# Kernel optimization log

Measured on AMD Instinct MI355X. Metric: run time of the kernel, lower is better.

## Reference

```python
import jax, jax.numpy as jnp
import numpy as np

B, V, T, C, HIN, WIN = 1, 6, 3, 256, 32, 32
NH = 8
LN_EPS = 1e-5


def setup_inputs() -> dict:
    key = jax.random.key(0)
    ks = jax.random.split(key, 14)
    s = 0.02
    lim = 1.0 / np.sqrt(C)
    def lin_w(k):
        return jax.random.uniform(k, (C, C), jnp.float32, -lim, lim)
    return {
        "history_feats": jax.random.normal(ks[0], (B, V, T, C, HIN, WIN), jnp.float32),
        "query_embed": jax.random.normal(ks[1], (1, C, 1, 1), jnp.float32) * s,
        "camera_pos_embed": jax.random.normal(ks[2], (V, C), jnp.float32) * s,
        "temporal_pos_embed": jax.random.normal(ks[3], (T, C), jnp.float32) * s,
        "spatial_pos_embed": jax.random.normal(ks[4], (1, C, 1, 1), jnp.float32) * s,
        "q_w": lin_w(ks[5]), "q_b": jnp.zeros((C,), jnp.float32),
        "k_w": lin_w(ks[6]), "k_b": jnp.zeros((C,), jnp.float32),
        "v_w": lin_w(ks[7]), "v_b": jnp.zeros((C,), jnp.float32),
        "o_w": lin_w(ks[8]), "o_b": jnp.zeros((C,), jnp.float32),
        "ln_g": jnp.ones((C,), jnp.float32),
        "ln_b": jnp.zeros((C,), jnp.float32),
        "query_cam_idx": 0,
        "H": 32,
        "W": 32,
    }


def reference(history_feats, query_embed, camera_pos_embed, temporal_pos_embed,
              spatial_pos_embed, q_w, q_b, k_w, k_b, v_w, v_b, o_w, o_b,
              ln_g, ln_b, query_cam_idx, H, W):
    B_, V_, T_, C_, Hin, Win = history_feats.shape
    dh = C_ // NH
    # --- build query: [B, H*W, C] ---
    q = query_embed + camera_pos_embed[query_cam_idx][None, :, None, None] + spatial_pos_embed
    q = jnp.broadcast_to(q, (B_, C_, H, W)).reshape(B_, C_, H * W).transpose(0, 2, 1)
    kv = (history_feats
          + temporal_pos_embed[None, None, :, :, None, None]
          + camera_pos_embed[None, :, None, :, None, None])
    kv = kv.transpose(0, 1, 2, 4, 5, 3).reshape(B_, V_ * T_ * Hin * Win, C_)
    # --- projections (torch Linear: x @ W.T + b) ---
    qp = q @ q_w.T + q_b
    kp = kv @ k_w.T + k_b
    vp = kv @ v_w.T + v_b
    # --- split heads: [B, NH, L, dh] ---
    qh = qp.reshape(B_, H * W, NH, dh).transpose(0, 2, 1, 3)
    kh = kp.reshape(B_, -1, NH, dh).transpose(0, 2, 1, 3)
    vh = vp.reshape(B_, -1, NH, dh).transpose(0, 2, 1, 3)
    scale = float(dh) ** -0.5
    attn = jax.nn.softmax(jnp.einsum('bhqd,bhkd->bhqk', qh, kh) * scale, axis=-1)
    out = jnp.einsum('bhqk,bhkd->bhqd', attn, vh)
    out = out.transpose(0, 2, 1, 3).reshape(B_, H * W, C_)
    out = out @ o_w.T + o_b
    # --- LayerNorm over channel dim ---
    mu = out.mean(-1, keepdims=True)
    var = ((out - mu) ** 2).mean(-1, keepdims=True)
    out = (out - mu) * jax.lax.rsqrt(var + LN_EPS) * ln_g + ln_b
    return out.transpose(0, 2, 1).reshape(B_, C_, H, W)
```

## Files before the change

### kernel.cpp

```cpp
#include <hip/hip_runtime.h>
#include <hip/hip_fp16.h>

typedef const float* fcp;

#define C_    256
#define NH_   8
#define DH_   32
#define VT_   18
#define HWK   1024
#define SCALE_ 0.17677669529663687f

#define QP_OFF   0
#define EMB_OFF  256
#define WF_OFF   4864
#define BB_OFF   6912
#define PS_OFF   6920
#define CTX_OFF  9224
#define B2_OFF   11272
#define Z_OFF    11528
#define SUM_OFF  11784
#define W2_OFF   12288

__device__ __forceinline__ float blockReduceSum256(float v){
  __shared__ float red[4];
  #pragma unroll
  for (int off = 32; off; off >>= 1) v += __shfl_xor(v, off, 64);
  const int lane = threadIdx.x & 63, w = threadIdx.x >> 6;
  __syncthreads();
  if (lane == 0) red[w] = v;
  __syncthreads();
  return red[0] + red[1] + red[2] + red[3];
}

__global__ void k_fold(fcp qe, fcp cam, fcp tpe, fcp spe, const int* __restrict__ cidx,
                       fcp qw, fcp qb, fcp kw, fcp kb, fcp vw, fcp vb, fcp ow, fcp ob,
                       float* __restrict__ ws){
  __shared__ float qvS[C_];
  __shared__ float qpS[DH_];
  __shared__ float owS[C_];
  const int b = blockIdx.x, t = threadIdx.x, lane = t & 63, wv = t >> 6;
  const int ci = cidx[0];
  qvS[t] = qe[t] + cam[ci*C_ + t] + spe[t];
  owS[t] = ow[(size_t)b*C_ + t];
  if (b < VT_){
    const int v = b/3, tt = b - v*3;
    ws[EMB_OFF + b*C_ + t] = tpe[tt*C_ + t] + cam[v*C_ + t];
  }
  if (b >= 18 && b < 26) ws[CTX_OFF + (b-18)*C_ + t] = 0.f;
  if (b == 26 && t < 2) ws[SUM_OFF + t] = 0.f;
  __syncthreads();
  if (b < 8){
    #pragma unroll
    for (int i = 0; i < 8; i++){
      const int r = b*DH_ + wv*8 + i;
      fcp qr = qw + (size_t)r*C_;
      float v = qr[lane]*qvS[lane] + qr[64+lane]*qvS[64+lane]
              + qr[128+lane]*qvS[128+lane] + qr[192+lane]*qvS[192+lane];
      #pragma unroll
      for (int off = 32; off; off >>= 1) v += __shfl_xor(v, off, 64);
      if (lane == 0) qpS[wv*8 + i] = v + qb[r];
    }
    __syncthreads();
    float acc = 0.f;
    #pragma unroll 8
    for (int d = 0; d < DH_; d++)
      acc += qpS[d] * kw[(size_t)(b*DH_ + d)*C_ + t];
    ws[WF_OFF + b*C_ + t] = SCALE_ * acc;
    if (t == 0){
      float bb = 0.f;
      for (int d = 0; d < DH_; d++) bb += qpS[d] * kb[b*DH_ + d];
      ws[BB_OFF + b] = SCALE_ * bb;
    }
  }
  {
    float acc[8] = {0,0,0,0,0,0,0,0};
    #pragma unroll 8
    for (int hd = 0; hd < 256; hd++){
      const float wsc = owS[hd];
      acc[hd >> 5] += wsc * vw[(size_t)hd*C_ + t];
    }
    float* wrow = ws + W2_OFF + (size_t)b*2048;
    #pragma unroll
    for (int h = 0; h < 8; h++) wrow[h*256 + t] = acc[h];
  }
  {
    float v2 = owS[t] * vb[t];
    v2 = blockReduceSum256(v2);
    if (t == 0) ws[B2_OFF + b] = v2 + ob[b];
  }
}

__global__ void k_attn(fcp feats, float* __restrict__ ws){
  __shared__ __align__(16) float wf[C_*8];
  __shared__ float redS[32];
  __shared__ float basef[8];
  __shared__ __align__(16) float pred[8*512];
  __shared__ float pexS[64*8];
  __shared__ __half fS[8*32*66];
  const int bid = blockIdx.x, vt = bid >> 4, sc = bid & 15, t = threadIdx.x;
  const int s = t & 63, cgi = t >> 6;

  for (int idx = t; idx < 2048; idx += 512){
    const int h = idx >> 8, c = idx & 255;
    wf[c*8 + h] = ws[WF_OFF + idx];
  }
  __syncthreads();
  if (t < 256){
    const float e = ws[EMB_OFF + vt*C_ + t];
    const float4 wa = *(const float4*)&wf[t*8];
    const float4 wb = *(const float4*)&wf[t*8 + 4];
    float pb[8] = {e*wa.x, e*wa.y, e*wa.z, e*wa.w, e*wb.x, e*wb.y, e*wb.z, e*wb.w};
    #pragma unroll
    for (int h = 0; h < 8; h++){
      float v = pb[h];
      #pragma unroll
      for (int off = 32; off; off >>= 1) v += __shfl_xor(v, off, 64);
      if ((t & 63) == 0) redS[(t >> 6)*8 + h] = v;
    }
  }
  __syncthreads();
  if (t < 8) basef[t] = redS[t] + redS[8+t] + redS[16+t] + redS[24+t] + ws[BB_OFF + t];
  __syncthreads();
  {
    fcp fp = feats + ((size_t)vt*C_ + cgi*32)*HWK + sc*64 + s;
    float acc[8] = {0,0,0,0,0,0,0,0};
    #pragma unroll 8
    for (int i = 0; i < 32; i++){
      const float fv = fp[(size_t)i*HWK];
      fS[(cgi*32 + i)*66 + s] = __float2half(fv);
      const float4 wa = *(const float4*)&wf[(cgi*32+i)*8];
      const float4 wb = *(const float4*)&wf[(cgi*32+i)*8 + 4];
      acc[0] += fv*wa.x; acc[1] += fv*wa.y; acc[2] += fv*wa.z; acc[3] += fv*wa.w;
      acc[4] += fv*wb.x; acc[5] += fv*wb.y; acc[6] += fv*wb.z; acc[7] += fv*wb.w;
    }
    #pragma unroll
    for (int h = 0; h < 8; h++) pred[cgi*512 + h*64 + s] = acc[h];
  }
  __syncthreads();
  {
    const int h1 = t >> 6, tok = t & 63;
    float sum = basef[h1];
    #pragma unroll
    for (int cg2 = 0; cg2 < 8; cg2++) sum += pred[cg2*512 + t];
    const float e = __expf(sum);
    pexS[tok*8 + h1] = e;
    float v = e;
    #pragma unroll
    for (int off = 32; off; off >>= 1) v += __shfl_xor(v, off, 64);
    if (tok == 0) ws[PS_OFF + bid*8 + h1] = v;
  }
  __syncthreads();
  {
    const int lane = t & 63, hB = lane & 7, isub = lane >> 3;
    float aB[4] = {0.f, 0.f, 0.f, 0.f};
    #pragma unroll 8
    for (int s2 = 0; s2 < 64; s2++){
      const float pe = pexS[s2*8 + hB];
      #pragma unroll
      for (int p = 0; p < 4; p++)
        aB[p] += pe * __half2float(fS[(cgi*32 + p*8 + isub)*66 + s2]);
    }
    #pragma unroll
    for (int p = 0; p < 4; p++)
      atomicAdd(ws + CTX_OFF + hB*256 + cgi*32 + p*8 + isub, aB[p]);
  }
}

__global__ void k_zproj(float* __restrict__ ws){
  __shared__ float psS[288*8];
  __shared__ float Ps[VT_*8];
  __shared__ float denomS[8];
  __shared__ __align__(16) float ctxnS[2048];
  const int o = blockIdx.x, t = threadIdx.x;
  for (int i = t; i < 288*8; i += 256) psS[i] = ws[PS_OFF + i];
  __syncthreads();
  if (t < VT_*8){
    const int vt = t >> 3, h = t & 7;
    float p = 0.f;
    #pragma unroll
    for (int s2 = 0; s2 < 16; s2++) p += psS[(vt*16 + s2)*8 + h];
    Ps[t] = p;
  }
  __syncthreads();
  if (t < 8){
    float d = 0.f;
    #pragma unroll
    for (int vt = 0; vt < VT_; vt++) d += Ps[vt*8 + t];
    denomS[t] = d;
  }
  __syncthreads();
  {
    float embP[8] = {0,0,0,0,0,0,0,0};
    #pragma unroll 2
    for (int vt = 0; vt < VT_; vt++){
      const float e = ws[EMB_OFF + vt*C_ + t];
      #pragma unroll
      for (int h = 0; h < 8; h++) embP[h] += e * Ps[vt*8 + h];
    }
    #pragma unroll
    for (int h = 0; h < 8; h++)
      ctxnS[h*256 + t] = (ws[CTX_OFF + h*256 + t] + embP[h]) / denomS[h];
  }
  __syncthreads();
  float v = 0.f;
  const float* wrow = ws + W2_OFF + (size_t)o*2048;
  #pragma unroll
  for (int k = 0; k < 8; k++) v += wrow[k*256 + t] * ctxnS[k*256 + t];
  v = blockReduceSum256(v);
  if (t == 0){
    const float z = v + ws[B2_OFF + o];
    ws[Z_OFF + o] = z;
    atomicAdd(ws + SUM_OFF, z);
    atomicAdd(ws + SUM_OFF + 1, z*z);
  }
}

__global__ void k_out(fcp lng, fcp lnb, const float* __restrict__ ws,
                      float* __restrict__ out, int hw){
  const int c = blockIdx.x, t = threadIdx.x;
  const float mu  = ws[SUM_OFF] * (1.f/C_);
  const float var = ws[SUM_OFF + 1] * (1.f/C_) - mu*mu;
  const float rs = rsqrtf(var + 1e-5f);
  const float fin = (ws[Z_OFF + c] - mu) * rs * lng[c] + lnb[c];
  float4 pk = make_float4(fin, fin, fin, fin);
  ((float4*)(out + (size_t)c*hw))[t] = pk;
}

extern "C" void kernel_launch(void* const* d_in, const int* in_sizes, int n_in,
                              void* d_out, int out_size, void* d_ws, size_t ws_size,
                              hipStream_t stream) {
  fcp feats = (fcp)d_in[0];
  fcp qe    = (fcp)d_in[1];
  fcp cam   = (fcp)d_in[2];
  fcp tpe   = (fcp)d_in[3];
  fcp spe   = (fcp)d_in[4];
  fcp qw    = (fcp)d_in[5];
  fcp qb    = (fcp)d_in[6];
  fcp kw    = (fcp)d_in[7];
  fcp kb    = (fcp)d_in[8];
  fcp vw    = (fcp)d_in[9];
  fcp vb    = (fcp)d_in[10];
  fcp ow    = (fcp)d_in[11];
  fcp ob    = (fcp)d_in[12];
  fcp lng   = (fcp)d_in[13];
  fcp lnb   = (fcp)d_in[14];
  const int* cidx = (const int*)d_in[15];
  float* ws = (float*)d_ws;
  float* out = (float*)d_out;
  const int hw = out_size / C_;

  k_fold <<<256, 256, 0, stream>>>(qe, cam, tpe, spe, cidx, qw, qb, kw, kb,
                                   vw, vb, ow, ob, ws);
  k_attn <<<288, 512, 0, stream>>>(feats, ws);
  k_zproj<<<256, 256, 0, stream>>>(ws);
  k_out  <<<256, 256, 0, stream>>>(lng, lnb, ws, out, hw);
}
```

Measured before the change: 152.4 us.

## Fuse attention, output projection and LayerNorm into one kernel with grid barriers

Merges the attention, z-projection and output kernels into a single persistent-style kernel that coordinates its phases through atomic counters and spin-wait grid barriers. Per-block context partials are written to workspace and reduced by 8 head blocks, replacing the float atomicAdd accumulation. This removes two kernel launches and their gaps. In exchange it adds spin-wait synchronization, which relies on all 288 blocks being co-resident to avoid deadlock. It also adds a serial 288-way reduction in only 8 blocks.

```diff
diff --git a/kernel.cpp b/kernel.cpp
--- a/kernel.cpp
+++ b/kernel.cpp
@@ -10,16 +10,16 @@
 #define HWK   1024
 #define SCALE_ 0.17677669529663687f
 
-#define QP_OFF   0
 #define EMB_OFF  256
 #define WF_OFF   4864
 #define BB_OFF   6912
 #define PS_OFF   6920
-#define CTX_OFF  9224
-#define B2_OFF   11272
-#define Z_OFF    11528
-#define SUM_OFF  11784
+#define B2_OFF   9224
+#define SUM_OFF  9480
+#define CNT_OFF  9482
+#define CTXN_OFF 9728
 #define W2_OFF   12288
+#define CTXP_OFF 536576
 
 __device__ __forceinline__ float blockReduceSum256(float v){
   __shared__ float red[4];
@@ -46,8 +46,8 @@
     const int v = b/3, tt = b - v*3;
     ws[EMB_OFF + b*C_ + t] = tpe[tt*C_ + t] + cam[v*C_ + t];
   }
-  if (b >= 18 && b < 26) ws[CTX_OFF + (b-18)*C_ + t] = 0.f;
   if (b == 26 && t < 2) ws[SUM_OFF + t] = 0.f;
+  if (b == 27 && t < 3) ((unsigned*)(ws + CNT_OFF))[t] = 0u;
   __syncthreads();
   if (b < 8){
     #pragma unroll
@@ -90,15 +90,22 @@
   }
 }
 
-__global__ void k_attn(fcp feats, float* __restrict__ ws){
+__global__ void __launch_bounds__(512, 4)
+k_main(fcp feats, fcp lng, fcp lnb, float* __restrict__ ws,
+       float* __restrict__ out, int hw){
   __shared__ __align__(16) float wf[C_*8];
   __shared__ float redS[32];
   __shared__ float basef[8];
   __shared__ __align__(16) float pred[8*512];
   __shared__ float pexS[64*8];
   __shared__ __half fS[8*32*66];
+  __shared__ float psR[288];
+  __shared__ float PvtR[VT_];
+  __shared__ float dR;
+  __shared__ float red8[8];
   const int bid = blockIdx.x, vt = bid >> 4, sc = bid & 15, t = threadIdx.x;
   const int s = t & 63, cgi = t >> 6;
+  unsigned* cnt = (unsigned*)(ws + CNT_OFF);
 
   for (int idx = t; idx < 2048; idx += 512){
     const int h = idx >> 8, c = idx & 255;
@@ -160,70 +167,99 @@
       for (int p = 0; p < 4; p++)
         aB[p] += pe * __half2float(fS[(cgi*32 + p*8 + isub)*66 + s2]);
     }
+    float* outp = ws + CTXP_OFF + (size_t)bid*2048;
     #pragma unroll
     for (int p = 0; p < 4; p++)
-      atomicAdd(ws + CTX_OFF + hB*256 + cgi*32 + p*8 + isub, aB[p]);
-  }
-}
-
-__global__ void k_zproj(float* __restrict__ ws){
-  __shared__ float psS[288*8];
-  __shared__ float Ps[VT_*8];
-  __shared__ float denomS[8];
-  __shared__ __align__(16) float ctxnS[2048];
-  const int o = blockIdx.x, t = threadIdx.x;
-  for (int i = t; i < 288*8; i += 256) psS[i] = ws[PS_OFF + i];
-  __syncthreads();
-  if (t < VT_*8){
-    const int vt = t >> 3, h = t & 7;
-    float p = 0.f;
-    #pragma unroll
-    for (int s2 = 0; s2 < 16; s2++) p += psS[(vt*16 + s2)*8 + h];
-    Ps[t] = p;
-  }
-  __syncthreads();
-  if (t < 8){
-    float d = 0.f;
-    #pragma unroll
-    for (int vt = 0; vt < VT_; vt++) d += Ps[vt*8 + t];
-    denomS[t] = d;
-  }
-  __syncthreads();
-  {
-    float embP[8] = {0,0,0,0,0,0,0,0};
-    #pragma unroll 2
-    for (int vt = 0; vt < VT_; vt++){
-      const float e = ws[EMB_OFF + vt*C_ + t];
-      #pragma unroll
-      for (int h = 0; h < 8; h++) embP[h] += e * Ps[vt*8 + h];
-    }
-    #pragma unroll
-    for (int h = 0; h < 8; h++)
-      ctxnS[h*256 + t] = (ws[CTX_OFF + h*256 + t] + embP[h]) / denomS[h];
-  }
-  __syncthreads();
+      outp[hB*256 + cgi*32 + p*8 + isub] = aB[p];
+  }
+  __threadfence();
+  __syncthreads();
+  if (t == 0) __hip_atomic_fetch_add(&cnt[0], 1u, __ATOMIC_RELEASE, __HIP_MEMORY_SCOPE_AGENT);
+  if (bid >= 256) return;
+
+  if (bid < 8){
+    if (t == 0){
+      while (__hip_atomic_load(&cnt[0], __ATOMIC_ACQUIRE, __HIP_MEMORY_SCOPE_AGENT) < 288u)
+        __builtin_amdgcn_s_sleep(2);
+    }
+    __syncthreads();
+    __threadfence();
+    const int h = bid;
+    if (t < 288) psR[t] = ws[PS_OFF + t*8 + h];
+    __syncthreads();
+    if (t < VT_){
+      float p = 0.f;
+      #pragma unroll
+      for (int j = 0; j < 16; j++) p += psR[t*16 + j];
+      PvtR[t] = p;
+    }
+    __syncthreads();
+    if (t == 0){
+      float d = 0.f;
+      #pragma unroll
+      for (int vt2 = 0; vt2 < VT_; vt2++) d += PvtR[vt2];
+      dR = d;
+    }
+    __syncthreads();
+    if (t < 256){
+      float ctx = 0.f;
+      const float* pp = ws + CTXP_OFF + h*256 + t;
+      #pragma unroll 8
+      for (int b2 = 0; b2 < 288; b2++) ctx += pp[(size_t)b2*2048];
+      float embP = 0.f;
+      #pragma unroll 2
+      for (int vt2 = 0; vt2 < VT_; vt2++) embP += ws[EMB_OFF + vt2*C_ + t] * PvtR[vt2];
+      ws[CTXN_OFF + h*256 + t] = (ctx + embP) / dR;
+    }
+    __threadfence();
+    __syncthreads();
+    if (t == 0) __hip_atomic_fetch_add(&cnt[1], 1u, __ATOMIC_RELEASE, __HIP_MEMORY_SCOPE_AGENT);
+  }
+
+  if (t == 0){
+    while (__hip_atomic_load(&cnt[1], __ATOMIC_ACQUIRE, __HIP_MEMORY_SCOPE_AGENT) < 8u)
+      __builtin_amdgcn_s_sleep(2);
+  }
+  __syncthreads();
+  __threadfence();
   float v = 0.f;
-  const float* wrow = ws + W2_OFF + (size_t)o*2048;
-  #pragma unroll
-  for (int k = 0; k < 8; k++) v += wrow[k*256 + t] * ctxnS[k*256 + t];
-  v = blockReduceSum256(v);
+  if (t < 256){
+    const float* wrow = ws + W2_OFF + (size_t)bid*2048;
+    const float* cn = ws + CTXN_OFF;
+    #pragma unroll
+    for (int k = 0; k < 8; k++) v += wrow[k*256 + t] * cn[k*256 + t];
+  }
+  {
+    #pragma unroll
+    for (int off = 32; off; off >>= 1) v += __shfl_xor(v, off, 64);
+    const int lane = t & 63, w = t >> 6;
+    __syncthreads();
+    if (lane == 0) red8[w] = v;
+    __syncthreads();
+    v = red8[0]+red8[1]+red8[2]+red8[3]+red8[4]+red8[5]+red8[6]+red8[7];
+  }
+  const float z = v + ws[B2_OFF + bid];
   if (t == 0){
-    const float z = v + ws[B2_OFF + o];
-    ws[Z_OFF + o] = z;
     atomicAdd(ws + SUM_OFF, z);
     atomicAdd(ws + SUM_OFF + 1, z*z);
-  }
-}
-
-__global__ void k_out(fcp lng, fcp lnb, const float* __restrict__ ws,
-                      float* __restrict__ out, int hw){
-  const int c = blockIdx.x, t = threadIdx.x;
-  const float mu  = ws[SUM_OFF] * (1.f/C_);
-  const float var = ws[SUM_OFF + 1] * (1.f/C_) - mu*mu;
+    __threadfence();
+    __hip_atomic_fetch_add(&cnt[2], 1u, __ATOMIC_RELEASE, __HIP_MEMORY_SCOPE_AGENT);
+    while (__hip_atomic_load(&cnt[2], __ATOMIC_ACQUIRE, __HIP_MEMORY_SCOPE_AGENT) < 256u)
+      __builtin_amdgcn_s_sleep(2);
+  }
+  __syncthreads();
+  __threadfence();
+
+  const float s1 = __hip_atomic_load(ws + SUM_OFF,     __ATOMIC_RELAXED, __HIP_MEMORY_SCOPE_AGENT);
+  const float s2 = __hip_atomic_load(ws + SUM_OFF + 1, __ATOMIC_RELAXED, __HIP_MEMORY_SCOPE_AGENT);
+  const float mu = s1 * (1.f/C_);
+  const float var = s2 * (1.f/C_) - mu*mu;
   const float rs = rsqrtf(var + 1e-5f);
-  const float fin = (ws[Z_OFF + c] - mu) * rs * lng[c] + lnb[c];
-  float4 pk = make_float4(fin, fin, fin, fin);
-  ((float4*)(out + (size_t)c*hw))[t] = pk;
+  if (t < 256){
+    const float fin = (z - mu) * rs * lng[bid] + lnb[bid];
+    float4 pk = make_float4(fin, fin, fin, fin);
+    ((float4*)(out + (size_t)bid*hw))[t] = pk;
+  }
 }
 
 extern "C" void kernel_launch(void* const* d_in, const int* in_sizes, int n_in,
@@ -251,7 +287,5 @@
 
   k_fold <<<256, 256, 0, stream>>>(qe, cam, tpe, spe, cidx, qw, qb, kw, kb,
                                    vw, vb, ow, ob, ws);
-  k_attn <<<288, 512, 0, stream>>>(feats, ws);
-  k_zproj<<<256, 256, 0, stream>>>(ws);
-  k_out  <<<256, 256, 0, stream>>>(lng, lnb, ws, out, hw);
-}
+  k_main <<<288, 512, 0, stream>>>(feats, lng, lnb, ws, out, hw);
+}
```

Measured after the change: 449.4 us. +194.9%, slower.
